# Optimization experiments

Hardware: AMD Instinct MI355X
Metric: run time of the kernel (lower is better)

Reference implementation:

```python
import jax, jax.numpy as jnp
from jax import lax
import numpy as np

# Keras LSTM cell semantics: gate order [i, f, c(candidate), o];
# recurrent_activation = sigmoid, activation = act (relu for all layers except
# the final decoder LSTM which uses tanh). h = o * act(c).

def lstm_layer(x, W, U, b, act, return_sequences):
    # x: [B, T, I], W: [I, 4H], U: [H, 4H], b: [4H]
    B = x.shape[0]
    H = U.shape[0]
    xW = jnp.einsum('bti,ih->bth', x, W) + b  # precompute input projections
    def step(carry, xw_t):
        h, c = carry
        z = xw_t + h @ U                      # [B, 4H]
        i, f, g, o = jnp.split(z, 4, axis=-1)
        i = jax.nn.sigmoid(i)
        f = jax.nn.sigmoid(f)
        g = act(g)
        o = jax.nn.sigmoid(o)
        c = f * c + i * g
        h = o * act(c)
        return (h, c), h
    h0 = jnp.zeros((B, H), x.dtype)
    (hT, _), hs = lax.scan(step, (h0, h0), jnp.swapaxes(xW, 0, 1))
    if return_sequences:
        return jnp.swapaxes(hs, 0, 1)         # [B, T, H]
    return hT                                  # [B, H]

# layer dims: (in, hidden) for enc0, enc1, enc_latent, dec0, dec1, dec_out
LAYER_DIMS = [(256, 512), (512, 256), (256, 64), (64, 256), (256, 512), (512, 256)]

def setup_inputs() -> dict:
    key = jax.random.key(0)
    keys = jax.random.split(key, 1 + 3 * len(LAYER_DIMS))
    inp = {'x': jax.random.normal(keys[0], (64, 256, 256), dtype=jnp.float32)}
    for li, (din, dh) in enumerate(LAYER_DIMS):
        kw, ku, _ = keys[1 + 3 * li], keys[2 + 3 * li], keys[3 + 3 * li]
        sW = 1.0 / np.sqrt(din)
        sU = 1.0 / np.sqrt(dh)
        inp[f'W{li}'] = jax.random.normal(kw, (din, 4 * dh), dtype=jnp.float32) * sW
        inp[f'U{li}'] = jax.random.normal(ku, (dh, 4 * dh), dtype=jnp.float32) * sU
        inp[f'b{li}'] = jnp.zeros((4 * dh,), dtype=jnp.float32)
    return inp

def reference(x, W0, U0, b0, W1, U1, b1, W2, U2, b2, W3, U3, b3, W4, U4, b4, W5, U5, b5):
    relu = jax.nn.relu
    # encoder: relu LSTMs, all return_sequences=True
    h = lstm_layer(x, W0, U0, b0, relu, True)
    h = lstm_layer(h, W1, U1, b1, relu, True)
    h = lstm_layer(h, W2, U2, b2, relu, True)   # latent_dim=64
    # decoder: relu LSTMs then final tanh LSTM with return_sequences=False
    h = lstm_layer(h, W3, U3, b3, relu, True)
    h = lstm_layer(h, W4, U4, b4, relu, True)
    out = lstm_layer(h, W5, U5, b5, jnp.tanh, False)  # [B, input_size]
    return out
```

## Files before the change

kernel.cpp:

```cpp
#include <hip/hip_runtime.h>
#include <stdint.h>

#define AGENT __HIP_MEMORY_SCOPE_AGENT
typedef unsigned long long u64;

__global__ __launch_bounds__(256) void xpose_in(const float* __restrict__ x,
                                                float* __restrict__ xT) {
  const int t = blockIdx.x;
  const int b = threadIdx.x & 63;
  const int w = threadIdx.x >> 6;
  const float* xr = x + ((size_t)b * 256 + t) * 256;
  float* o = xT + (size_t)t * 256 * 64;
  for (int kq = w * 16; kq < w * 16 + 16; ++kq) {
    float4 v = *(const float4*)(xr + kq * 4);
    o[(size_t)(kq * 4 + 0) * 64 + b] = v.x;
    o[(size_t)(kq * 4 + 1) * 64 + b] = v.y;
    o[(size_t)(kq * 4 + 2) * 64 + b] = v.z;
    o[(size_t)(kq * 4 + 3) * 64 + b] = v.w;
  }
}

__global__ __launch_bounds__(256) void pack_wu(const float* __restrict__ W,
                                               const float* __restrict__ U,
                                               float* __restrict__ out,
                                               int DIN, int H) {
  __shared__ float tile[64][65];
  const int KT = DIN + H;
  const int KTq = KT >> 2;
  const int c0 = blockIdx.x * 64;
  const int k0 = blockIdx.y * 64;
  const int tx = threadIdx.x & 63;
  const int ty = threadIdx.x >> 6;
  for (int r = ty; r < 64; r += 4) {
    const int k = k0 + r;
    tile[r][tx] = (k < DIN) ? W[(size_t)k * (4 * H) + c0 + tx]
                            : U[(size_t)(k - DIN) * (4 * H) + c0 + tx];
  }
  __syncthreads();
  for (int r = ty; r < 64; r += 4) {
    const int cg = c0 + r;
    const int g = cg / H;
    const int col = cg - g * H;
    const int wg = col >> 2;
    const int jl = col & 3;
    const int c = (g << 2) | jl;
    const int k = k0 + tx;
    const int q = k >> 2;
    const int j = k & 3;
    out[(((size_t)wg * KTq + q) * 16 + c) * 4 + j] = tile[tx][r];
  }
}

#define SB __builtin_amdgcn_sched_barrier(0)
#define FMA_B8(I_, WS_, XA_, XB_)                                   \
  acc[(I_) * 8 + 0] = fmaf(WS_, (XA_).x, acc[(I_) * 8 + 0]);        \
  acc[(I_) * 8 + 1] = fmaf(WS_, (XA_).y, acc[(I_) * 8 + 1]);        \
  acc[(I_) * 8 + 2] = fmaf(WS_, (XA_).z, acc[(I_) * 8 + 2]);        \
  acc[(I_) * 8 + 3] = fmaf(WS_, (XA_).w, acc[(I_) * 8 + 3]);        \
  acc[(I_) * 8 + 4] = fmaf(WS_, (XB_).x, acc[(I_) * 8 + 4]);        \
  acc[(I_) * 8 + 5] = fmaf(WS_, (XB_).y, acc[(I_) * 8 + 5]);        \
  acc[(I_) * 8 + 6] = fmaf(WS_, (XB_).z, acc[(I_) * 8 + 6]);        \
  acc[(I_) * 8 + 7] = fmaf(WS_, (XB_).w, acc[(I_) * 8 + 7]);
#define FMA_ROW32(I_, WV_)                 \
  FMA_B8(I_, (WV_).x, x0a_, x0b_)          \
  FMA_B8(I_, (WV_).y, x1a_, x1b_)          \
  FMA_B8(I_, (WV_).z, x2a_, x2b_)          \
  FMA_B8(I_, (WV_).w, x3a_, x3b_)

template <int QL>
__device__ __forceinline__ void accum88(const float4* __restrict__ sp,
                                        const float4* __restrict__ wp,
                                        float acc[64]) {
#pragma unroll 1
  for (int q = 0; q < QL; ++q) {
    const float4 x0a_ = sp[0],  x0b_ = sp[1];
    const float4 x1a_ = sp[16], x1b_ = sp[17];
    const float4 x2a_ = sp[32], x2b_ = sp[33];
    const float4 x3a_ = sp[48], x3b_ = sp[49];
    const float4 w0_ = wp[0], w1_ = wp[1], w2_ = wp[2], w3_ = wp[3];
    const float4 w4_ = wp[4], w5_ = wp[5], w6_ = wp[6], w7_ = wp[7];
    FMA_ROW32(0, w0_)
    FMA_ROW32(1, w1_)
    FMA_ROW32(2, w2_)
    FMA_ROW32(3, w3_)
    FMA_ROW32(4, w4_)
    FMA_ROW32(5, w5_)
    FMA_ROW32(6, w6_)
    FMA_ROW32(7, w7_)
    SB;
    sp += 64;
    wp += 17;
  }
}

template <int NWG>
__device__ __forceinline__ void agg_body(unsigned* __restrict__ flg,
                                         unsigned* __restrict__ ep) {
  const int tid = threadIdx.x;
  if (tid >= 64) return;
  for (int t = 0; t < 256; ++t) {
    unsigned* base = flg + (size_t)t * NWG;
    if (NWG <= 64) {
      if (tid < NWG) {
        while (__hip_atomic_load(base + tid, __ATOMIC_RELAXED, AGENT) == 0u)
          __builtin_amdgcn_s_sleep(1);
      }
    } else {
      while (__hip_atomic_load(base + tid, __ATOMIC_RELAXED, AGENT) == 0u)
        __builtin_amdgcn_s_sleep(1);
      while (__hip_atomic_load(base + 64 + tid, __ATOMIC_RELAXED, AGENT) == 0u)
        __builtin_amdgcn_s_sleep(1);
    }
    asm volatile("s_waitcnt vmcnt(0)" ::: "memory");
    if (tid == 0)
      __hip_atomic_store(ep, (unsigned)(t + 1), __ATOMIC_RELAXED, AGENT);
  }
}

template <int DIN, int H, int NWG, bool FIN, bool XCOH>
__device__ __forceinline__ void layer_body(
    int wg, int tid, const float* __restrict__ xin, float* __restrict__ hseq,
    const float* __restrict__ wP, const float* __restrict__ bias,
    float* __restrict__ dout, unsigned* __restrict__ selfF,
    unsigned* __restrict__ selfE, unsigned* __restrict__ prevE,
    float* __restrict__ wL, float (*sZ)[16][64], float* sH) {
  constexpr int KT = DIN + H;
  constexpr int KTq = KT / 4;
  constexpr int XQ4 = DIN / 4;
  constexpr int QLX = DIN / 64;
  constexpr int QLH = H / 64;
  constexpr int SLABX = QLX * 17 + 2;
  constexpr int SLABH = QLH * 17 + 2;
  constexpr int T = 256;
  static_assert(DIN % 64 == 0 && H % 64 == 0, "16-way K-slicing");

  const int lane = tid & 63;
  const int wv = tid >> 6;
  const int cq = lane >> 5;
  const int k4 = (lane >> 3) & 3;
  const int bq = lane & 7;
  const int slice = wv * 4 + k4;

  {
    float4* wl = (float4*)wL;
    const float4* wp = (const float4*)wP + (size_t)wg * KTq * 16;
    for (int i = tid; i < KTq * 16; i += 256) {
      const int qg = i >> 4;
      const int c = i & 15;
      int lidx;
      if (qg < XQ4) {
        lidx = (qg / QLX) * SLABX + (qg % QLX) * 17 + c + (c >> 3);
      } else {
        const int qh = qg - XQ4;
        lidx = 16 * SLABX + (qh / QLH) * SLABH + (qh % QLH) * 17 + c + (c >> 3);
      }
      wl[lidx] = wp[i];
    }
  }
  const float4* wbx = (const float4*)wL + (size_t)slice * SLABX + cq * 9;
  const float4* wbh =
      (const float4*)wL + (size_t)16 * SLABX + (size_t)slice * SLABH + cq * 9;

  float bz[4];
#pragma unroll
  for (int g = 0; g < 4; ++g) bz[g] = bias[g * H + wg * 4 + wv];
  float cst = 0.f;
  __syncthreads();

  for (int t = 0; t < T; ++t) {
    float acc[64];
#pragma unroll
    for (int c = 0; c < 64; ++c) acc[c] = 0.f;

    if (!XCOH) {
      accum88<QLX>((const float4*)(xin + (size_t)t * DIN * 64) +
                       (size_t)slice * QLX * 64 + bq * 2,
                   wbx, acc);
    }
    if (t > 0 && tid == 0) {
      while (__hip_atomic_load(selfE, __ATOMIC_RELAXED, AGENT) < (unsigned)t)
        __builtin_amdgcn_s_sleep(2);
    }
    if (XCOH && tid == 64) {
      while (__hip_atomic_load(prevE, __ATOMIC_RELAXED, AGENT) <
             (unsigned)(t + 1))
        __builtin_amdgcn_s_sleep(2);
    }
    __syncthreads();
    asm volatile("" ::: "memory");

    if (XCOH) {
      accum88<QLX>((const float4*)(xin + (size_t)t * DIN * 64) +
                       (size_t)slice * QLX * 64 + bq * 2,
                   wbx, acc);
    }
    if (t > 0) {
      accum88<QLH>((const float4*)(hseq + (size_t)(t - 1) * H * 64) +
                       (size_t)slice * QLH * 64 + bq * 2,
                   wbh, acc);
    }

#pragma unroll
    for (int r = 0; r < 64; ++r) {
      const int v = __builtin_amdgcn_ds_swizzle(__float_as_int(acc[r]),
                                                0x201F);
      acc[r] += __int_as_float(v);
    }
#pragma unroll
    for (int r = 0; r < 64; ++r) {
      const int v = __builtin_amdgcn_ds_swizzle(__float_as_int(acc[r]),
                                                0x401F);
      acc[r] += __int_as_float(v);
    }

    if (k4 == 0) {
#pragma unroll
      for (int i = 0; i < 8; ++i) {
#pragma unroll
        for (int h = 0; h < 2; ++h) {
          *(float4*)&sZ[wv][cq * 8 + i][bq * 8 + h * 4] =
              make_float4(acc[i * 8 + h * 4 + 0], acc[i * 8 + h * 4 + 1],
                          acc[i * 8 + h * 4 + 2], acc[i * 8 + h * 4 + 3]);
        }
      }
    }
    __syncthreads();

    float z[4];
#pragma unroll
    for (int g = 0; g < 4; ++g) {
      z[g] = bz[g];
#pragma unroll
      for (int k = 0; k < 4; ++k) z[g] += sZ[k][g * 4 + wv][lane];
    }
    const float ig = 1.f / (1.f + __expf(-z[0]));
    const float fg = 1.f / (1.f + __expf(-z[1]));
    const float gg = FIN ? tanhf(z[2]) : fmaxf(z[2], 0.f);
    const float og = 1.f / (1.f + __expf(-z[3]));
    cst = fg * cst + ig * gg;
    const float ca = FIN ? tanhf(cst) : fmaxf(cst, 0.f);
    const float h = og * ca;
    sH[lane * 4 + wv] = h;
    if (FIN && t == T - 1) dout[(size_t)lane * H + wg * 4 + wv] = h;
    __syncthreads();

    if (wv == 0) {
      float* hw = hseq + (size_t)t * H * 64 + (size_t)(wg * 4) * 64 + lane;
#pragma unroll
      for (int jl = 0; jl < 4; ++jl) {
        __hip_atomic_store(hw + jl * 64, sH[lane * 4 + jl], __ATOMIC_RELAXED,
                           AGENT);
      }
      asm volatile("s_waitcnt vmcnt(0)" ::: "memory");
      if (tid == 0)
        __hip_atomic_store(&selfF[t * NWG + wg], 1u, __ATOMIC_RELAXED, AGENT);
    }
  }
}

__global__ __launch_bounds__(256, 2) void lstm_fused(
    const float* __restrict__ xT, float* __restrict__ h0,
    float* __restrict__ h1, float* __restrict__ h2, float* __restrict__ h3,
    float* __restrict__ h4, float* __restrict__ h5,
    const float* __restrict__ wuT0, const float* __restrict__ wuT1,
    const float* __restrict__ wuT2, const float* __restrict__ wuT3,
    const float* __restrict__ wuT4, const float* __restrict__ wuT5,
    const float* __restrict__ b0, const float* __restrict__ b1,
    const float* __restrict__ b2, const float* __restrict__ b3,
    const float* __restrict__ b4, const float* __restrict__ b5,
    float* __restrict__ dout, unsigned* __restrict__ f0,
    unsigned* __restrict__ f1, unsigned* __restrict__ f2,
    unsigned* __restrict__ f3, unsigned* __restrict__ f4,
    unsigned* __restrict__ f5, unsigned* __restrict__ eps) {
  __shared__ alignas(16) float wLDS[4 * 3328];
  __shared__ alignas(16) float sZ[4][16][64];
  __shared__ alignas(16) float sH[256];
  const int b = blockIdx.x;
  const int tid = threadIdx.x;
  if (b < 128) {
    layer_body<256, 512, 128, false, false>(b, tid, xT, h0, wuT0, b0, nullptr,
                                            f0, eps + 0, nullptr, wLDS, sZ, sH);
  } else if (b < 256) {
    layer_body<256, 512, 128, false, true>(b - 128, tid, h3, h4, wuT4, b4,
                                           nullptr, f4, eps + 4, eps + 3, wLDS,
                                           sZ, sH);
  } else if (b < 320) {
    layer_body<512, 256, 64, false, true>(b - 256, tid, h0, h1, wuT1, b1,
                                          nullptr, f1, eps + 1, eps + 0, wLDS,
                                          sZ, sH);
  } else if (b < 384) {
    layer_body<64, 256, 64, false, true>(b - 320, tid, h2, h3, wuT3, b3,
                                         nullptr, f3, eps + 3, eps + 2, wLDS,
                                         sZ, sH);
  } else if (b < 448) {
    layer_body<512, 256, 64, true, true>(b - 384, tid, h4, h5, wuT5, b5, dout,
                                         f5, eps + 5, eps + 4, wLDS, sZ, sH);
  } else if (b < 464) {
    layer_body<256, 64, 16, false, true>(b - 448, tid, h1, h2, wuT2, b2,
                                         nullptr, f2, eps + 2, eps + 1, wLDS,
                                         sZ, sH);
  } else {
    const int l = b - 464;
    if (l == 0) agg_body<128>(f0, eps + 0);
    else if (l == 1) agg_body<64>(f1, eps + 1);
    else if (l == 2) agg_body<16>(f2, eps + 2);
    else if (l == 3) agg_body<64>(f3, eps + 3);
    else if (l == 4) agg_body<128>(f4, eps + 4);
    else agg_body<64>(f5, eps + 5);
  }
}

extern "C" void kernel_launch(void* const* d_in, const int* in_sizes, int n_in,
                              void* d_out, int out_size, void* d_ws,
                              size_t ws_size, hipStream_t stream) {
  (void)in_sizes; (void)n_in; (void)out_size; (void)ws_size;
  const float* x = (const float*)d_in[0];
  const float* W[6];
  const float* U[6];
  const float* B[6];
  for (int l = 0; l < 6; ++l) {
    W[l] = (const float*)d_in[1 + 3 * l];
    U[l] = (const float*)d_in[2 + 3 * l];
    B[l] = (const float*)d_in[3 + 3 * l];
  }
  char* ws = (char*)d_ws;
  unsigned* f0 = (unsigned*)ws;
  unsigned* f1 = f0 + 128 * 256;
  unsigned* f2 = f1 + 64 * 256;
  unsigned* f3 = f2 + 16 * 256;
  unsigned* f4 = f3 + 64 * 256;
  unsigned* f5 = f4 + 128 * 256;
  unsigned* eps = f0 + 464 * 256;
  float* wuT0 = (float*)(ws + (1u << 20));
  float* wuT1 = wuT0 + (size_t)2048 * 768;
  float* wuT2 = wuT1 + (size_t)1024 * 768;
  float* wuT3 = wuT2 + (size_t)256 * 320;
  float* wuT4 = wuT3 + (size_t)1024 * 320;
  float* wuT5 = wuT4 + (size_t)2048 * 768;
  float* xT = (float*)(ws + (22u << 20));
  float* h0 = (float*)(ws + (38u << 20));
  float* h1 = (float*)(ws + (70u << 20));
  float* h2 = (float*)(ws + (86u << 20));
  float* h3 = (float*)(ws + (90u << 20));
  float* h4 = (float*)(ws + (106u << 20));
  float* h5 = (float*)(ws + (138u << 20));

  hipMemsetAsync(f0, 0, (464 * 256 + 8) * sizeof(unsigned), stream);
  xpose_in<<<256, 256, 0, stream>>>(x, xT);
  pack_wu<<<dim3(32, 12), 256, 0, stream>>>(W[0], U[0], wuT0, 256, 512);
  pack_wu<<<dim3(16, 12), 256, 0, stream>>>(W[1], U[1], wuT1, 512, 256);
  pack_wu<<<dim3(4, 5), 256, 0, stream>>>(W[2], U[2], wuT2, 256, 64);
  pack_wu<<<dim3(16, 5), 256, 0, stream>>>(W[3], U[3], wuT3, 64, 256);
  pack_wu<<<dim3(32, 12), 256, 0, stream>>>(W[4], U[4], wuT4, 256, 512);
  pack_wu<<<dim3(16, 12), 256, 0, stream>>>(W[5], U[5], wuT5, 512, 256);

  lstm_fused<<<470, 256, 0, stream>>>(xT, h0, h1, h2, h3, h4, h5, wuT0, wuT1,
                                      wuT2, wuT3, wuT4, wuT5, B[0], B[1], B[2],
                                      B[3], B[4], B[5], (float*)d_out, f0, f1,
                                      f2, f3, f4, f5, eps);
}
```

Baseline: 3.371 ms.

## Use 16x8 register tile with 32-way K split for 768-wide LSTM layers

```diff
diff --git a/kernel.cpp b/kernel.cpp
--- a/kernel.cpp
+++ b/kernel.cpp
@@ -66,6 +66,25 @@
   FMA_B8(I_, (WV_).y, x1a_, x1b_)          \
   FMA_B8(I_, (WV_).z, x2a_, x2b_)          \
   FMA_B8(I_, (WV_).w, x3a_, x3b_)
+#define QUAD_FMA(SPQ_, WPQ_)                                        \
+  {                                                                 \
+    const float4 x0a_ = (SPQ_)[0], x0b_ = (SPQ_)[1];                \
+    const float4 x1a_ = (SPQ_)[16], x1b_ = (SPQ_)[17];              \
+    const float4 x2a_ = (SPQ_)[32], x2b_ = (SPQ_)[33];              \
+    const float4 x3a_ = (SPQ_)[48], x3b_ = (SPQ_)[49];              \
+    const float4 w0_ = (WPQ_)[0], w1_ = (WPQ_)[1];                  \
+    const float4 w2_ = (WPQ_)[2], w3_ = (WPQ_)[3];                  \
+    const float4 w4_ = (WPQ_)[4], w5_ = (WPQ_)[5];                  \
+    const float4 w6_ = (WPQ_)[6], w7_ = (WPQ_)[7];                  \
+    FMA_ROW32(0, w0_)                                               \
+    FMA_ROW32(1, w1_)                                               \
+    FMA_ROW32(2, w2_)                                               \
+    FMA_ROW32(3, w3_)                                               \
+    FMA_ROW32(4, w4_)                                               \
+    FMA_ROW32(5, w5_)                                               \
+    FMA_ROW32(6, w6_)                                               \
+    FMA_ROW32(7, w7_)                                               \
+  }
 
 template <int QL>
 __device__ __forceinline__ void accum88(const float4* __restrict__ sp,
@@ -73,23 +92,51 @@
                                         float acc[64]) {
 #pragma unroll 1
   for (int q = 0; q < QL; ++q) {
-    const float4 x0a_ = sp[0],  x0b_ = sp[1];
+    QUAD_FMA(sp, wp)
+    SB;
+    sp += 64;
+    wp += 17;
+  }
+}
+
+template <int QL>
+__device__ __forceinline__ void accum168(const float4* __restrict__ sp,
+                                         const float4* __restrict__ wp,
+                                         float acc[128]) {
+#pragma unroll 1
+  for (int q = 0; q < QL; ++q) {
+    const float4 x0a_ = sp[0], x0b_ = sp[1];
     const float4 x1a_ = sp[16], x1b_ = sp[17];
     const float4 x2a_ = sp[32], x2b_ = sp[33];
     const float4 x3a_ = sp[48], x3b_ = sp[49];
-    const float4 w0_ = wp[0], w1_ = wp[1], w2_ = wp[2], w3_ = wp[3];
-    const float4 w4_ = wp[4], w5_ = wp[5], w6_ = wp[6], w7_ = wp[7];
-    FMA_ROW32(0, w0_)
-    FMA_ROW32(1, w1_)
-    FMA_ROW32(2, w2_)
-    FMA_ROW32(3, w3_)
-    FMA_ROW32(4, w4_)
-    FMA_ROW32(5, w5_)
-    FMA_ROW32(6, w6_)
-    FMA_ROW32(7, w7_)
+    {
+      const float4 w0_ = wp[0], w1_ = wp[1], w2_ = wp[2], w3_ = wp[3];
+      const float4 w4_ = wp[4], w5_ = wp[5], w6_ = wp[6], w7_ = wp[7];
+      FMA_ROW32(0, w0_)
+      FMA_ROW32(1, w1_)
+      FMA_ROW32(2, w2_)
+      FMA_ROW32(3, w3_)
+      FMA_ROW32(4, w4_)
+      FMA_ROW32(5, w5_)
+      FMA_ROW32(6, w6_)
+      FMA_ROW32(7, w7_)
+    }
+    SB;
+    {
+      const float4 w0_ = wp[8], w1_ = wp[9], w2_ = wp[10], w3_ = wp[11];
+      const float4 w4_ = wp[12], w5_ = wp[13], w6_ = wp[14], w7_ = wp[15];
+      FMA_ROW32(8, w0_)
+      FMA_ROW32(9, w1_)
+      FMA_ROW32(10, w2_)
+      FMA_ROW32(11, w3_)
+      FMA_ROW32(12, w4_)
+      FMA_ROW32(13, w5_)
+      FMA_ROW32(14, w6_)
+      FMA_ROW32(15, w7_)
+    }
     SB;
     sp += 64;
-    wp += 17;
+    wp += 16;
   }
 }
 
@@ -124,22 +171,21 @@
     float* __restrict__ dout, unsigned* __restrict__ selfF,
     unsigned* __restrict__ selfE, unsigned* __restrict__ prevE,
     float* __restrict__ wL, float (*sZ)[16][64], float* sH) {
-  constexpr int KT = DIN + H;
-  constexpr int KTq = KT / 4;
+  constexpr bool WIDE = (DIN + H == 768);
+  constexpr int KTq = (DIN + H) / 4;
   constexpr int XQ4 = DIN / 4;
-  constexpr int QLX = DIN / 64;
-  constexpr int QLH = H / 64;
-  constexpr int SLABX = QLX * 17 + 2;
-  constexpr int SLABH = QLH * 17 + 2;
   constexpr int T = 256;
-  static_assert(DIN % 64 == 0 && H % 64 == 0, "16-way K-slicing");
+  constexpr int WQLX = WIDE ? DIN / 128 : 1;
+  constexpr int WQLH = WIDE ? H / 128 : 1;
+  constexpr int WSLABX = WQLX * 16 + 1;
+  constexpr int WSLABH = WQLH * 16 + 1;
+  constexpr int LQLX = DIN / 64;
+  constexpr int LQLH = H / 64;
+  constexpr int LSLABX = LQLX * 17 + 2;
+  constexpr int LSLABH = LQLH * 17 + 2;
 
   const int lane = tid & 63;
   const int wv = tid >> 6;
-  const int cq = lane >> 5;
-  const int k4 = (lane >> 3) & 3;
-  const int bq = lane & 7;
-  const int slice = wv * 4 + k4;
 
   {
     float4* wl = (float4*)wL;
@@ -148,18 +194,25 @@
       const int qg = i >> 4;
       const int c = i & 15;
       int lidx;
-      if (qg < XQ4) {
-        lidx = (qg / QLX) * SLABX + (qg % QLX) * 17 + c + (c >> 3);
+      if constexpr (WIDE) {
+        if (qg < XQ4) {
+          lidx = (qg / WQLX) * WSLABX + (qg % WQLX) * 16 + c;
+        } else {
+          const int qh = qg - XQ4;
+          lidx = 32 * WSLABX + (qh / WQLH) * WSLABH + (qh % WQLH) * 16 + c;
+        }
       } else {
-        const int qh = qg - XQ4;
-        lidx = 16 * SLABX + (qh / QLH) * SLABH + (qh % QLH) * 17 + c + (c >> 3);
+        if (qg < XQ4) {
+          lidx = (qg / LQLX) * LSLABX + (qg % LQLX) * 17 + c + (c >> 3);
+        } else {
+          const int qh = qg - XQ4;
+          lidx =
+              16 * LSLABX + (qh / LQLH) * LSLABH + (qh % LQLH) * 17 + c + (c >> 3);
+        }
       }
       wl[lidx] = wp[i];
     }
   }
-  const float4* wbx = (const float4*)wL + (size_t)slice * SLABX + cq * 9;
-  const float4* wbh =
-      (const float4*)wL + (size_t)16 * SLABX + (size_t)slice * SLABH + cq * 9;
 
   float bz[4];
 #pragma unroll
@@ -167,93 +220,206 @@
   float cst = 0.f;
   __syncthreads();
 
-  for (int t = 0; t < T; ++t) {
-    float acc[64];
-#pragma unroll
-    for (int c = 0; c < 64; ++c) acc[c] = 0.f;
-
-    if (!XCOH) {
-      accum88<QLX>((const float4*)(xin + (size_t)t * DIN * 64) +
-                       (size_t)slice * QLX * 64 + bq * 2,
-                   wbx, acc);
+  if constexpr (WIDE) {
+    const int k8 = lane & 7;
+    const int bq = lane >> 3;
+    const int slice = wv * 8 + k8;
+    const float4* wbx = (const float4*)wL + (size_t)slice * WSLABX;
+    const float4* wbh =
+        (const float4*)wL + (size_t)32 * WSLABX + (size_t)slice * WSLABH;
+
+    for (int t = 0; t < T; ++t) {
+      float acc[128];
+#pragma unroll
+      for (int c = 0; c < 128; ++c) acc[c] = 0.f;
+
+      if (!XCOH) {
+        accum168<WQLX>((const float4*)(xin + (size_t)t * DIN * 64) +
+                           (size_t)slice * WQLX * 64 + bq * 2,
+                       wbx, acc);
+      }
+      if (t > 0 && tid == 0) {
+        while (__hip_atomic_load(selfE, __ATOMIC_RELAXED, AGENT) < (unsigned)t)
+          __builtin_amdgcn_s_sleep(2);
+      }
+      if (XCOH && tid == 64) {
+        while (__hip_atomic_load(prevE, __ATOMIC_RELAXED, AGENT) <
+               (unsigned)(t + 1))
+          __builtin_amdgcn_s_sleep(2);
+      }
+      __syncthreads();
+      asm volatile("" ::: "memory");
+
+      if (XCOH) {
+        accum168<WQLX>((const float4*)(xin + (size_t)t * DIN * 64) +
+                           (size_t)slice * WQLX * 64 + bq * 2,
+                       wbx, acc);
+      }
+      if (t > 0) {
+        accum168<WQLH>((const float4*)(hseq + (size_t)(t - 1) * H * 64) +
+                           (size_t)slice * WQLH * 64 + bq * 2,
+                       wbh, acc);
+      }
+
+#pragma unroll
+      for (int r = 0; r < 128; ++r) {
+        const int v = __builtin_amdgcn_update_dpp(0, __float_as_int(acc[r]),
+                                                  0xB1, 0xF, 0xF, false);
+        acc[r] += __int_as_float(v);
+      }
+#pragma unroll
+      for (int r = 0; r < 128; ++r) {
+        const int v = __builtin_amdgcn_update_dpp(0, __float_as_int(acc[r]),
+                                                  0x4E, 0xF, 0xF, false);
+        acc[r] += __int_as_float(v);
+      }
+#pragma unroll
+      for (int r = 0; r < 128; ++r) {
+        const int v =
+            __builtin_amdgcn_ds_swizzle(__float_as_int(acc[r]), 0x101F);
+        acc[r] += __int_as_float(v);
+      }
+
+      if (k8 == 0) {
+#pragma unroll
+        for (int i = 0; i < 16; ++i) {
+#pragma unroll
+          for (int h = 0; h < 2; ++h) {
+            *(float4*)&sZ[wv][i][bq * 8 + h * 4] =
+                make_float4(acc[i * 8 + h * 4 + 0], acc[i * 8 + h * 4 + 1],
+                            acc[i * 8 + h * 4 + 2], acc[i * 8 + h * 4 + 3]);
+          }
+        }
+      }
+      __syncthreads();
+
+      float z[4];
+#pragma unroll
+      for (int g = 0; g < 4; ++g) {
+        z[g] = bz[g];
+#pragma unroll
+        for (int k = 0; k < 4; ++k) z[g] += sZ[k][g * 4 + wv][lane];
+      }
+      const float ig = 1.f / (1.f + __expf(-z[0]));
+      const float fg = 1.f / (1.f + __expf(-z[1]));
+      const float gg = FIN ? tanhf(z[2]) : fmaxf(z[2], 0.f);
+      const float og = 1.f / (1.f + __expf(-z[3]));
+      cst = fg * cst + ig * gg;
+      const float ca = FIN ? tanhf(cst) : fmaxf(cst, 0.f);
+      const float h = og * ca;
+      sH[lane * 4 + wv] = h;
+      if (FIN && t == T - 1) dout[(size_t)lane * H + wg * 4 + wv] = h;
+      __syncthreads();
+
+      if (wv == 0) {
+        float* hw = hseq + (size_t)t * H * 64 + (size_t)(wg * 4) * 64 + lane;
+#pragma unroll
+        for (int jl = 0; jl < 4; ++jl) {
+          __hip_atomic_store(hw + jl * 64, sH[lane * 4 + jl], __ATOMIC_RELAXED,
+                             AGENT);
+        }
+        asm volatile("s_waitcnt vmcnt(0)" ::: "memory");
+        if (tid == 0)
+          __hip_atomic_store(&selfF[t * NWG + wg], 1u, __ATOMIC_RELAXED, AGENT);
+      }
     }
-    if (t > 0 && tid == 0) {
-      while (__hip_atomic_load(selfE, __ATOMIC_RELAXED, AGENT) < (unsigned)t)
-        __builtin_amdgcn_s_sleep(2);
-    }
-    if (XCOH && tid == 64) {
-      while (__hip_atomic_load(prevE, __ATOMIC_RELAXED, AGENT) <
-             (unsigned)(t + 1))
-        __builtin_amdgcn_s_sleep(2);
-    }
-    __syncthreads();
-    asm volatile("" ::: "memory");
-
-    if (XCOH) {
-      accum88<QLX>((const float4*)(xin + (size_t)t * DIN * 64) +
-                       (size_t)slice * QLX * 64 + bq * 2,
-                   wbx, acc);
-    }
-    if (t > 0) {
-      accum88<QLH>((const float4*)(hseq + (size_t)(t - 1) * H * 64) +
-                       (size_t)slice * QLH * 64 + bq * 2,
-                   wbh, acc);
-    }
-
-#pragma unroll
-    for (int r = 0; r < 64; ++r) {
-      const int v = __builtin_amdgcn_ds_swizzle(__float_as_int(acc[r]),
-                                                0x201F);
-      acc[r] += __int_as_float(v);
-    }
-#pragma unroll
-    for (int r = 0; r < 64; ++r) {
-      const int v = __builtin_amdgcn_ds_swizzle(__float_as_int(acc[r]),
-                                                0x401F);
-      acc[r] += __int_as_float(v);
-    }
-
-    if (k4 == 0) {
-#pragma unroll
-      for (int i = 0; i < 8; ++i) {
-#pragma unroll
-        for (int h = 0; h < 2; ++h) {
-          *(float4*)&sZ[wv][cq * 8 + i][bq * 8 + h * 4] =
-              make_float4(acc[i * 8 + h * 4 + 0], acc[i * 8 + h * 4 + 1],
-                          acc[i * 8 + h * 4 + 2], acc[i * 8 + h * 4 + 3]);
+  } else {
+    const int cq = lane >> 5;
+    const int k4 = (lane >> 3) & 3;
+    const int bq = lane & 7;
+    const int slice = wv * 4 + k4;
+    const float4* wbx = (const float4*)wL + (size_t)slice * LSLABX + cq * 9;
+    const float4* wbh = (const float4*)wL + (size_t)16 * LSLABX +
+                        (size_t)slice * LSLABH + cq * 9;
+
+    for (int t = 0; t < T; ++t) {
+      float acc[64];
+#pragma unroll
+      for (int c = 0; c < 64; ++c) acc[c] = 0.f;
+
+      if (!XCOH) {
+        accum88<LQLX>((const float4*)(xin + (size_t)t * DIN * 64) +
+                          (size_t)slice * LQLX * 64 + bq * 2,
+                      wbx, acc);
+      }
+      if (t > 0 && tid == 0) {
+        while (__hip_atomic_load(selfE, __ATOMIC_RELAXED, AGENT) < (unsigned)t)
+          __builtin_amdgcn_s_sleep(2);
+      }
+      if (XCOH && tid == 64) {
+        while (__hip_atomic_load(prevE, __ATOMIC_RELAXED, AGENT) <
+               (unsigned)(t + 1))
+          __builtin_amdgcn_s_sleep(2);
+      }
+      __syncthreads();
+      asm volatile("" ::: "memory");
+
+      if (XCOH) {
+        accum88<LQLX>((const float4*)(xin + (size_t)t * DIN * 64) +
+                          (size_t)slice * LQLX * 64 + bq * 2,
+                      wbx, acc);
+      }
+      if (t > 0) {
+        accum88<LQLH>((const float4*)(hseq + (size_t)(t - 1) * H * 64) +
+                          (size_t)slice * LQLH * 64 + bq * 2,
+                      wbh, acc);
+      }
+
+#pragma unroll
+      for (int r = 0; r < 64; ++r) {
+        const int v = __builtin_amdgcn_ds_swizzle(__float_as_int(acc[r]),
+                                                  0x201F);
+        acc[r] += __int_as_float(v);
+      }
+#pragma unroll
+      for (int r = 0; r < 64; ++r) {
+        const int v = __builtin_amdgcn_ds_swizzle(__float_as_int(acc[r]),
+                                                  0x401F);
+        acc[r] += __int_as_float(v);
+      }
+
+      if (k4 == 0) {
+#pragma unroll
+        for (int i = 0; i < 8; ++i) {
+#pragma unroll
+          for (int h = 0; h < 2; ++h) {
+            *(float4*)&sZ[wv][cq * 8 + i][bq * 8 + h * 4] =
+                make_float4(acc[i * 8 + h * 4 + 0], acc[i * 8 + h * 4 + 1],
+                            acc[i * 8 + h * 4 + 2], acc[i * 8 + h * 4 + 3]);
+          }
         }
       }
-    }
-    __syncthreads();
-
-    float z[4];
-#pragma unroll
-    for (int g = 0; g < 4; ++g) {
-      z[g] = bz[g];
-#pragma unroll
-      for (int k = 0; k < 4; ++k) z[g] += sZ[k][g * 4 + wv][lane];
-    }
-    const float ig = 1.f / (1.f + __expf(-z[0]));
-    const float fg = 1.f / (1.f + __expf(-z[1]));
-    const float gg = FIN ? tanhf(z[2]) : fmaxf(z[2], 0.f);
-    const float og = 1.f / (1.f + __expf(-z[3]));
-    cst = fg * cst + ig * gg;
-    const float ca = FIN ? tanhf(cst) : fmaxf(cst, 0.f);
-    const float h = og * ca;
-    sH[lane * 4 + wv] = h;
-    if (FIN && t == T - 1) dout[(size_t)lane * H + wg * 4 + wv] = h;
-    __syncthreads();
-
-    if (wv == 0) {
-      float* hw = hseq + (size_t)t * H * 64 + (size_t)(wg * 4) * 64 + lane;
-#pragma unroll
-      for (int jl = 0; jl < 4; ++jl) {
-        __hip_atomic_store(hw + jl * 64, sH[lane * 4 + jl], __ATOMIC_RELAXED,
-                           AGENT);
-      }
-      asm volatile("s_waitcnt vmcnt(0)" ::: "memory");
-      if (tid == 0)
-        __hip_atomic_store(&selfF[t * NWG + wg], 1u, __ATOMIC_RELAXED, AGENT);
+      __syncthreads();
+
+      float z[4];
+#pragma unroll
+      for (int g = 0; g < 4; ++g) {
+        z[g] = bz[g];
+#pragma unroll
+        for (int k = 0; k < 4; ++k) z[g] += sZ[k][g * 4 + wv][lane];
+      }
+      const float ig = 1.f / (1.f + __expf(-z[0]));
+      const float fg = 1.f / (1.f + __expf(-z[1]));
+      const float gg = FIN ? tanhf(z[2]) : fmaxf(z[2], 0.f);
+      const float og = 1.f / (1.f + __expf(-z[3]));
+      cst = fg * cst + ig * gg;
+      const float ca = FIN ? tanhf(cst) : fmaxf(cst, 0.f);
+      const float h = og * ca;
+      sH[lane * 4 + wv] = h;
+      if (FIN && t == T - 1) dout[(size_t)lane * H + wg * 4 + wv] = h;
+      __syncthreads();
+
+      if (wv == 0) {
+        float* hw = hseq + (size_t)t * H * 64 + (size_t)(wg * 4) * 64 + lane;
+#pragma unroll
+        for (int jl = 0; jl < 4; ++jl) {
+          __hip_atomic_store(hw + jl * 64, sH[lane * 4 + jl], __ATOMIC_RELAXED,
+                             AGENT);
+        }
+        asm volatile("s_waitcnt vmcnt(0)" ::: "memory");
+        if (tid == 0)
+          __hip_atomic_store(&selfF[t * NWG + wg], 1u, __ATOMIC_RELAXED, AGENT);
+      }
     }
   }
 }
```

Measured after the change: 5.045 ms. +49.6%, slower.
